# Kernel tuning notes

Hardware: AMD Instinct MI355X
Metric: run time of the kernel (lower is better)

The kernel has to match this reference:

```python
import jax, jax.numpy as jnp
import numpy as np

B, LV, LT, D, H = 32, 196, 40, 512, 8
DH = D // H


def setup_inputs() -> dict:
    key = jax.random.key(0)
    ks = jax.random.split(key, 10)
    s = 0.02
    return {
        "bef_feat": jax.random.normal(ks[0], (B, LV, D), jnp.float32),
        "sent_feat": jax.random.normal(ks[1], (B, LT, D), jnp.float32),
        "aft_feat": jax.random.normal(ks[2], (B, LV, D), jnp.float32),
        "masks": jnp.ones((B, LT), jnp.float32),
        "conv1_w": jax.random.normal(ks[3], (D, 2 * D), jnp.float32) * s,  # 1x1 conv: (out,in)
        "conv1_b": jnp.zeros((D,), jnp.float32),
        "in_proj_w": jax.random.normal(ks[4], (3 * D, D), jnp.float32) * s,
        "out_proj_w": jax.random.normal(ks[5], (D, D), jnp.float32) * s,
        "conv2_w": jax.random.normal(ks[6], (D, D), jnp.float32) * s,
        "conv2_b": jnp.zeros((D,), jnp.float32),
        "q_w": jax.random.normal(ks[7], (D, D), jnp.float32) * s,
        "q_b": jnp.zeros((D,), jnp.float32),
        "k_w": jax.random.normal(ks[8], (D, D), jnp.float32) * s,
        "k_b": jnp.zeros((D,), jnp.float32),
        "logit_scale": jnp.ones((), jnp.float32),
    }


def _forward(bef_feat, sent_feat, aft_feat, masks,
             conv1_w, conv1_b, in_proj_w, out_proj_w, conv2_w, conv2_b,
             q_w, q_b, k_w, k_b, logit_scale):
    batch, Lv, d = bef_feat.shape
    # masked text mean (plain mean over full length, as in original)
    sent = sent_feat * masks[:, :, None]
    sent_mean = jnp.mean(sent, axis=1)  # (B, D)
    # concat image grid feat with broadcast text feat -> 1x1 conv (conv1)
    img = jnp.transpose(bef_feat, (0, 2, 1))                       # (B, D, 196)
    txt = jnp.broadcast_to(sent_mean[:, :, None], (batch, d, Lv))  # (B, D, 196)
    v1 = jnp.concatenate([img, txt], axis=1)                       # (B, 2D, 196)
    v1 = jnp.einsum('bcl,oc->blo', v1, conv1_w) + conv1_b          # (B, 196, D)
    # multi-head self-attention over the 196 positions (no biases)
    qkv = jnp.einsum('bld,ed->ble', v1, in_proj_w)                 # (B, 196, 3D)
    q, k, v = jnp.split(qkv, 3, axis=-1)
    to_heads = lambda t: t.reshape(batch, Lv, H, DH).transpose(0, 2, 1, 3)
    q, k, v = to_heads(q), to_heads(k), to_heads(v)
    scores = jnp.einsum('bhld,bhmd->bhlm', q, k) / jnp.sqrt(jnp.float32(DH))
    attn = jax.nn.softmax(scores, axis=-1)
    o = jnp.einsum('bhlm,bhmd->bhld', attn, v)
    o = o.transpose(0, 2, 1, 3).reshape(batch, Lv, d)
    o = o @ out_proj_w.T
    # 1x1 conv (conv2)
    mod_img1 = jnp.einsum('bld,od->blo', o, conv2_w) + conv2_b     # (B, 196, D)
    # ContraAttention: cross-batch retrieval logits
    ql = (mod_img1 @ q_w.T + q_b).reshape(batch, Lv, H, DH).transpose(0, 2, 1, 3)  # (B,H,196,DH)
    kl = (aft_feat @ k_w.T + k_b).reshape(batch, Lv, H, DH).transpose(0, 2, 1, 3)  # (B,H,196,DH)
    logits = jnp.einsum('ahld,bhmd->ablm', ql, kl)                 # (B, B, 196, 196), sums over h,d
    # vid_mask and com_mask (attention_mask) are all-ones -> sums are Lv
    t2v = jnp.sum(jnp.max(logits, axis=-1), axis=2) / jnp.float32(Lv)  # (B, B)
    v2t = jnp.sum(jnp.max(logits, axis=-2), axis=2) / jnp.float32(Lv)  # (B, B)
    S = 0.5 * (t2v + v2t) * jnp.exp(logit_scale)
    cross_en = lambda m: -jnp.mean(jnp.diag(jax.nn.log_softmax(m, axis=-1)))
    return 0.5 * (cross_en(S) + cross_en(S.T))


def reference(bef_feat, sent_feat, aft_feat, masks,
              conv1_w, conv1_b, in_proj_w, out_proj_w, conv2_w, conv2_b,
              q_w, q_b, k_w, k_b, logit_scale):
    return _forward(bef_feat, sent_feat, aft_feat, masks,
                    conv1_w, conv1_b, in_proj_w, out_proj_w, conv2_w, conv2_b,
                    q_w, q_b, k_w, k_b, logit_scale)
```

## Files before the change

### kernel.cpp

```cpp
#include <hip/hip_runtime.h>


typedef unsigned int u32;
typedef unsigned short u16;
typedef __attribute__((ext_vector_type(8))) short bf16x8;
typedef __attribute__((ext_vector_type(4))) float f32x4;

#define DEV __device__ __forceinline__

DEV u16 f2bf(float f) {
  u32 u = __builtin_bit_cast(u32, f);
  u = (u + 0x7FFFu + ((u >> 16) & 1u)) >> 16;
  return (u16)u;
}
DEV float bf2f(u16 h) { u32 u = ((u32)h) << 16; return __builtin_bit_cast(float, u); }
DEV u32 encf(float f) { u32 u = __builtin_bit_cast(u32, f); return (u & 0x80000000u) ? ~u : (u | 0x80000000u); }
DEV float decf(u32 e) { u32 u = (e & 0x80000000u) ? (e & 0x7FFFFFFFu) : ~e; return __builtin_bit_cast(float, u); }

DEV void gll16(const u16* g, u16* l) {
  __builtin_amdgcn_global_load_lds(
      (const __attribute__((address_space(1))) void*)g,
      (__attribute__((address_space(3))) void*)l, 16, 0, 0);
}

#define VMCNT0 asm volatile("s_waitcnt vmcnt(0)" ::: "memory")
#define SBAR __builtin_amdgcn_s_barrier()

DEV void cast8(const float* __restrict__ in, u16* __restrict__ out, int i) {
  const float4* p = (const float4*)in + (size_t)i * 2;
  float4 a = p[0], b = p[1];
  u16 t[8] = {f2bf(a.x), f2bf(a.y), f2bf(a.z), f2bf(a.w),
              f2bf(b.x), f2bf(b.y), f2bf(b.z), f2bf(b.w)};
  *(uint4*)(out + (size_t)i * 8) = *(uint4*)t;
}

DEV void tcast(const float* __restrict__ in, u16* __restrict__ out, int t, int tid, float* sm) {
  int bx = t & 15, by = t >> 4;
  int tx = tid & 31, ty = tid >> 5;
  float (*tt)[33] = (float(*)[33])sm;
  for (int i = ty; i < 32; i += 8) tt[i][tx] = in[(size_t)(by * 32 + i) * 512 + bx * 32 + tx];
  __syncthreads();
  for (int i = ty; i < 32; i += 8) out[(size_t)(bx * 32 + i) * 512 + by * 32 + tx] = f2bf(tt[tx][i]);
}

__global__ __launch_bounds__(256) void k_prep(
    const float* __restrict__ bef, const float* __restrict__ aft,
    const float* __restrict__ sent, const float* __restrict__ masks,
    const float* __restrict__ conv1_w, const float* __restrict__ conv1_b,
    const float* __restrict__ in_proj_w, const float* __restrict__ out_proj_w,
    const float* __restrict__ conv2_w, const float* __restrict__ conv2_b,
    const float* __restrict__ q_w, const float* __restrict__ q_b,
    const float* __restrict__ k_w,
    u16* __restrict__ bef16, u16* __restrict__ aft16,
    u16* __restrict__ inproj16, u16* __restrict__ kw16, u16* __restrict__ qw16,
    u16* __restrict__ w1a16, u16* __restrict__ wcT16, u16* __restrict__ woT16,
    float* __restrict__ biasb, float* __restrict__ biasq,
    uint4* __restrict__ maxbuf) {
  __shared__ float smemf[1056];
  const int blk = blockIdx.x, tid = threadIdx.x;
  if (blk < 32) {
    int b = blk;
    float* sm = smemf;
    for (int d = tid; d < 512; d += 256) {
      float s = 0.f;
#pragma unroll 8
      for (int t = 0; t < 40; ++t) s += sent[(size_t)b * 40 * 512 + (size_t)t * 512 + d] * masks[b * 40 + t];
      sm[d] = s * (1.0f / 40.0f);
    }
    __syncthreads();
    for (int o = tid; o < 512; o += 256) {
      const float* wr = conv1_w + (size_t)o * 1024 + 512;
      float acc = conv1_b[o];
#pragma unroll 8
      for (int c = 0; c < 512; ++c) acc += sm[c] * wr[c];
      biasb[b * 512 + o] = acc;
    }
  } else if (blk < 424) {
    maxbuf[(size_t)(blk - 32) * 256 + tid] = (uint4){0u, 0u, 0u, 0u};
  } else if (blk < 426) {
    int j = (blk - 424) * 256 + tid;
    if (j < 512) {
      const float* wr = q_w + (size_t)j * 512;
      float acc = q_b[j];
#pragma unroll 8
      for (int d = 0; d < 512; ++d) acc += wr[d] * conv2_b[d];
      biasq[j] = acc;
    }
  } else if (blk < 1994) {
    cast8(bef, bef16, (blk - 426) * 256 + tid);
  } else if (blk < 3562) {
    cast8(aft, aft16, (blk - 1994) * 256 + tid);
  } else if (blk < 3946) {
    cast8(in_proj_w, inproj16, (blk - 3562) * 256 + tid);
  } else if (blk < 4074) {
    cast8(k_w, kw16, (blk - 3946) * 256 + tid);
  } else if (blk < 4202) {
    cast8(q_w, qw16, (blk - 4074) * 256 + tid);
  } else if (blk < 4330) {
    int i = (blk - 4202) * 256 + tid;
    int o = i >> 6, c0 = (i & 63) * 8;
    const float* p = conv1_w + (size_t)o * 1024 + c0;
    u16 t[8];
#pragma unroll
    for (int j = 0; j < 8; ++j) t[j] = f2bf(p[j]);
    *(uint4*)(w1a16 + (size_t)o * 512 + c0) = *(uint4*)t;
  } else if (blk < 4586) {
    tcast(conv2_w, wcT16, blk - 4330, tid, smemf);
  } else {
    tcast(out_proj_w, woT16, blk - 4586, tid, smemf);
  }
}

DEV void stage_g3(const u16* __restrict__ xb, const u16* __restrict__ wb,
                  u16* Xb, u16* Wb, int wave, int lane, int koff, int scol) {
  int r8 = lane >> 3;
#pragma unroll
  for (int i = 0; i < 8; ++i) {
    int s = wave + i * 4;
    if (s < 16) gll16(xb + (size_t)(s * 8 + r8) * 512 + koff + scol, Xb + s * 512);
    else        gll16(wb + (size_t)((s - 16) * 8 + r8) * 512 + koff + scol, Wb + (s - 16) * 512);
  }
}

DEV void comp_g3(const u16* Xb, const u16* Wb, int wr, int wc, int quad, int l15, int rsw,
                 f32x4 (&acc)[4][4]) {
#pragma unroll
  for (int kk = 0; kk < 64; kk += 32) {
    int co = (kk | (quad << 3)) ^ rsw;
    bf16x8 af[4];
#pragma unroll
    for (int s = 0; s < 4; ++s)
      af[s] = *(const bf16x8*)&Xb[(wr * 64 + s * 16 + l15) * 64 + co];
#pragma unroll
    for (int nt = 0; nt < 4; ++nt) {
      bf16x8 b = *(const bf16x8*)&Wb[(wc * 64 + nt * 16 + l15) * 64 + co];
#pragma unroll
      for (int s = 0; s < 4; ++s)
        acc[s][nt] = __builtin_amdgcn_mfma_f32_16x16x32_bf16(af[s], b, acc[s][nt], 0, 0, 0);
    }
  }
}

__global__ __launch_bounds__(256) void k_gemm3d(
    const u16* __restrict__ X1, const u16* __restrict__ W1, u16* __restrict__ o1,
    const float* __restrict__ b1, int nbx1, int N1, int m1, int nblk1,
    const u16* __restrict__ X2, const u16* __restrict__ W2, u16* __restrict__ o2,
    const float* __restrict__ b2, int nbx2, int N2, int m2) {
  __shared__ u16 Xl0[128 * 64], Xl1[128 * 64];
  __shared__ u16 Wl0[128 * 64], Wl1[128 * 64];
  int g = blockIdx.x;
  const u16 *X, *W; u16* out; const float* bias; int N, biasMode, bx, by;
  if (g < nblk1) {
    X = X1; W = W1; out = o1; bias = b1; N = N1; biasMode = m1;
    bx = g % nbx1; by = g / nbx1;
  } else {
    g -= nblk1;
    X = X2; W = W2; out = o2; bias = b2; N = N2; biasMode = m2;
    bx = g % nbx2; by = g / nbx2;
  }
  int tid = threadIdx.x;
  int tileM = bx * 128, tileN = by * 128;
  int wave = tid >> 6, lane = tid & 63, quad = lane >> 4, l15 = lane & 15;
  int wr = wave >> 1, wc = wave & 1;
  const int rsw = (l15 & 7) << 3;
  const int scol = (((lane & 7) ^ ((lane >> 3) & 7)) << 3);
  f32x4 z = {0.f, 0.f, 0.f, 0.f};
  f32x4 acc[4][4];
#pragma unroll
  for (int s = 0; s < 4; ++s)
#pragma unroll
    for (int nt = 0; nt < 4; ++nt) acc[s][nt] = z;
  const u16* xb = X + (size_t)tileM * 512;
  const u16* wb = W + (size_t)tileN * 512;

  stage_g3(xb, wb, Xl0, Wl0, wave, lane, 0, scol);
  VMCNT0; SBAR;
#pragma unroll
  for (int kc = 0; kc < 8; kc += 2) {
    stage_g3(xb, wb, Xl1, Wl1, wave, lane, (kc + 1) * 64, scol);
    comp_g3(Xl0, Wl0, wr, wc, quad, l15, rsw, acc);
    VMCNT0; SBAR;
    if (kc + 2 < 8)
      stage_g3(xb, wb, Xl0, Wl0, wave, lane, (kc + 2) * 64, scol);
    comp_g3(Xl1, Wl1, wr, wc, quad, l15, rsw, acc);
    VMCNT0; SBAR;
  }
#pragma unroll
  for (int s = 0; s < 4; ++s) {
    int row0 = tileM + wr * 64 + s * 16 + quad * 4;
#pragma unroll
    for (int nt = 0; nt < 4; ++nt) {
      int col = tileN + wc * 64 + nt * 16 + l15;
      float bv = (biasMode == 1) ? bias[col] : 0.0f;
#pragma unroll
      for (int r = 0; r < 4; ++r) {
        int row = row0 + r;
        float v = acc[s][nt][r] + bv;
        if (biasMode == 2) v += bias[(row / 196) * 512 + col];
        out[(size_t)row * N + col] = f2bf(v);
      }
    }
  }
}

__global__ __launch_bounds__(256, 1) void k_attn2(const u16* __restrict__ qkv, u16* __restrict__ o_out) {
  const int blk = blockIdx.x;
  const int b = blk >> 4, h = (blk >> 1) & 7, half = blk & 1;
  const int sb = half * 8, se = half ? 13 : 8;
  __shared__ u16 Ks[208 * 72];
  __shared__ u16 Vt[64 * 232];
  __shared__ u16 Ps[4][16 * 232];
  const int tid = threadIdx.x;
  const int wave = tid >> 6, lane = tid & 63, quad = lane >> 4, l15 = lane & 15;
  const size_t base = (size_t)b * 196 * 1536 + (size_t)h * 64;

  for (int i = tid; i < 64 * 232 / 4; i += 256) ((unsigned long long*)Vt)[i] = 0ULL;
  for (int i = tid; i < 4 * 16 * 24; i += 256) {
    int w = i / 384, rem = i - w * 384;
    int r = rem / 24, c = rem - r * 24;
    Ps[w][r * 232 + 208 + c] = 0;
  }
  __syncthreads();

  for (int idx = tid; idx < 208 * 8; idx += 256) {
    int r = idx >> 3, c = (idx & 7) * 8;
    uint4 v = {0, 0, 0, 0};
    if (r < 196) v = *(const uint4*)&qkv[base + 512 + (size_t)r * 1536 + c];
    *(uint4*)&Ks[r * 72 + c] = v;
  }
  for (int idx = tid; idx < 196 * 8; idx += 256) {
    int p = idx >> 3, f0 = (idx & 7) * 8;
    uint4 v = *(const uint4*)&qkv[base + 1024 + (size_t)p * 1536 + f0];
    u16 t[8]; *(uint4*)t = v;
#pragma unroll
    for (int j = 0; j < 8; ++j) Vt[(f0 + j) * 232 + p] = t[j];
  }
  bf16x8 qz = {0, 0, 0, 0, 0, 0, 0, 0};
  bf16x8 qf[2][2];
#pragma unroll
  for (int i = 0; i < 2; ++i) {
    int s = sb + wave + i * 4;
    int row = s * 16 + l15;
#pragma unroll
    for (int c = 0; c < 2; ++c) {
      bf16x8 v = qz;
      if (s < se && row < 196)
        v = *(const bf16x8*)&qkv[base + (size_t)row * 1536 + c * 32 + quad * 8];
      qf[i][c] = v;
    }
  }
  __syncthreads();

  const f32x4 z = {0.f, 0.f, 0.f, 0.f};
  for (int i = 0; i < 2; ++i) {
    int s = sb + wave + i * 4;
    if (s >= se) break;
    f32x4 acc[13];
#pragma unroll
    for (int nt = 0; nt < 13; ++nt) acc[nt] = z;
#pragma unroll
    for (int c = 0; c < 2; ++c) {
      bf16x8 a = qf[i][c];
#pragma unroll
      for (int nt = 0; nt < 13; ++nt) {
        bf16x8 bfr = *(const bf16x8*)&Ks[(nt * 16 + l15) * 72 + c * 32 + quad * 8];
        acc[nt] = __builtin_amdgcn_mfma_f32_16x16x32_bf16(a, bfr, acc[nt], 0, 0, 0);
      }
    }
#pragma unroll
    for (int r = 0; r < 4; ++r) {
      float m = -3e38f;
#pragma unroll
      for (int nt = 0; nt < 13; ++nt) {
        float sv = acc[nt][r] * 0.125f;
        acc[nt][r] = sv;
        if (nt < 12 || l15 < 4) m = fmaxf(m, sv);
      }
#pragma unroll
      for (int off = 1; off < 16; off <<= 1) m = fmaxf(m, __shfl_xor(m, off));
      float ssum = 0.f;
#pragma unroll
      for (int nt = 0; nt < 13; ++nt) {
        float p = (nt < 12 || l15 < 4) ? __expf(acc[nt][r] - m) : 0.f;
        acc[nt][r] = p;
        ssum += p;
      }
#pragma unroll
      for (int off = 1; off < 16; off <<= 1) ssum += __shfl_xor(ssum, off);
      float is = 1.0f / ssum;
      int row = quad * 4 + r;
#pragma unroll
      for (int nt = 0; nt < 13; ++nt) {
        float v = acc[nt][r] * is;
        float vx = __shfl_xor(v, 1);
        if ((l15 & 1) == 0) {
          u32 pk = (u32)f2bf(v) | ((u32)f2bf(vx) << 16);
          *(u32*)&Ps[wave][row * 232 + nt * 16 + l15] = pk;
        }
      }
    }
    f32x4 oacc[4] = {z, z, z, z};
#pragma unroll
    for (int kc = 0; kc < 7; ++kc) {
      bf16x8 a = *(const bf16x8*)&Ps[wave][l15 * 232 + kc * 32 + quad * 8];
#pragma unroll
      for (int nt = 0; nt < 4; ++nt) {
        bf16x8 bfr = *(const bf16x8*)&Vt[(nt * 16 + l15) * 232 + kc * 32 + quad * 8];
        oacc[nt] = __builtin_amdgcn_mfma_f32_16x16x32_bf16(a, bfr, oacc[nt], 0, 0, 0);
      }
    }
#pragma unroll
    for (int nt = 0; nt < 4; ++nt) {
#pragma unroll
      for (int r = 0; r < 4; ++r) {
        int row = s * 16 + quad * 4 + r;
        if (row < 196)
          o_out[((size_t)b * 196 + row) * 512 + h * 64 + nt * 16 + l15] = f2bf(oacc[nt][r]);
      }
    }
  }
}

DEV void stage_lg(const u16* __restrict__ qbase, const u16* __restrict__ kbase,
                  u16* Qb, u16* Kb, int wave, int lane, int koff, int scol) {
  int r4 = lane >> 2;
#pragma unroll
  for (int i = 0; i < 6; ++i) {
    int s = wave + i * 4;
    if (s < 8) {
      gll16(qbase + (size_t)(s * 16 + r4) * 512 + koff + scol, Qb + s * 512);
    } else if (s < 21) {
      int j = s - 8;
      int r = j * 16 + r4; if (r > 195) r = 195;
      gll16(kbase + (size_t)r * 512 + koff + scol, Kb + j * 512);
    }
  }
}

DEV void comp_lg(const u16* Qb, const u16* Kb, int wave, int l15, int co, f32x4 (&acc)[2][13]) {
  bf16x8 af0 = *(const bf16x8*)&Qb[(wave * 16 + l15) * 32 + co];
  bf16x8 af1 = *(const bf16x8*)&Qb[((wave + 4) * 16 + l15) * 32 + co];
  __builtin_amdgcn_s_setprio(1);
#pragma unroll
  for (int nt = 0; nt < 13; ++nt) {
    bf16x8 b = *(const bf16x8*)&Kb[(nt * 16 + l15) * 32 + co];
    acc[0][nt] = __builtin_amdgcn_mfma_f32_16x16x32_bf16(af0, b, acc[0][nt], 0, 0, 0);
    acc[1][nt] = __builtin_amdgcn_mfma_f32_16x16x32_bf16(af1, b, acc[1][nt], 0, 0, 0);
  }
  __builtin_amdgcn_s_setprio(0);
}

#define WAIT_W() do { \
    if (wave == 0) asm volatile("s_waitcnt vmcnt(6)" ::: "memory"); \
    else           asm volatile("s_waitcnt vmcnt(5)" ::: "memory"); \
  } while (0)

__global__ __launch_bounds__(256) void k_logits2(const u16* __restrict__ QL, const u16* __restrict__ KL,
                                                 u32* __restrict__ rowmax, u32* __restrict__ colmax) {
  int lin = blockIdx.y * 49 + blockIdx.x;
  lin = (lin & 7) * 196 + (lin >> 3);
  const int bx = lin % 49, b = lin / 49;
  const int row0 = bx * 128;
  __shared__ u16 Qb0[128 * 32], Qb1[128 * 32], Qb2[128 * 32];
  __shared__ u16 Kb0[208 * 32], Kb1[208 * 32], Kb2[208 * 32];
  __shared__ float colred[2][4 * 208];
  const int tid = threadIdx.x;
  const int wave = tid >> 6, lane = tid & 63, quad = lane >> 4, l15 = lane & 15;
  const int scol = (((lane & 3) ^ ((lane >> 3) & 3)) << 3);
  const int co = ((quad ^ ((l15 >> 1) & 3)) << 3);
  const int a0 = row0 / 196;
  const int lsplit = (a0 + 1) * 196 - row0;
  const f32x4 z = {0.f, 0.f, 0.f, 0.f};
  f32x4 acc[2][13];
#pragma unroll
  for (int s = 0; s < 2; ++s)
#pragma unroll
    for (int nt = 0; nt < 13; ++nt) acc[s][nt] = z;
  const u16* qbase = QL + (size_t)row0 * 512;
  const u16* kbase = KL + (size_t)b * 196 * 512;

  u16 *qa = Qb0, *qb = Qb1, *qc = Qb2;
  u16 *ka = Kb0, *kb = Kb1, *kc = Kb2;
  stage_lg(qbase, kbase, qa, ka, wave, lane, 0, scol);
  stage_lg(qbase, kbase, qb, kb, wave, lane, 32, scol);
  for (int t = 0; t < 14; ++t) {
    WAIT_W();
    SBAR;
    stage_lg(qbase, kbase, qc, kc, wave, lane, (t + 2) * 32, scol);
    comp_lg(qa, ka, wave, l15, co, acc);
    u16* tq = qa; qa = qb; qb = qc; qc = tq;
    u16* tk = ka; ka = kb; kb = kc; kc = tk;
  }
  WAIT_W(); SBAR;
  comp_lg(qa, ka, wave, l15, co, acc);
  { u16* tq = qa; qa = qb; qb = qc; qc = tq;
    u16* tk = ka; ka = kb; kb = kc; kc = tk; }
  VMCNT0; SBAR;
  comp_lg(qa, ka, wave, l15, co, acc);

#pragma unroll
  for (int s = 0; s < 2; ++s) {
#pragma unroll
    for (int r = 0; r < 4; ++r) {
      float m = -3e38f;
#pragma unroll
      for (int nt = 0; nt < 13; ++nt)
        if (nt < 12 || l15 < 4) m = fmaxf(m, acc[s][nt][r]);
#pragma unroll
      for (int off = 8; off > 0; off >>= 1) m = fmaxf(m, __shfl_xor(m, off, 16));
      if (l15 == 0) {
        int lr = (wave + s * 4) * 16 + quad * 4 + r;
        int aa = a0, ll = row0 - a0 * 196 + lr;
        if (ll >= 196) { aa += 1; ll -= 196; }
        atomicMax(&rowmax[((size_t)aa * 32 + b) * 196 + ll], encf(m));
      }
    }
  }
#pragma unroll
  for (int nt = 0; nt < 13; ++nt) {
    float cm0 = -3e38f, cm1 = -3e38f;
#pragma unroll
    for (int s = 0; s < 2; ++s)
#pragma unroll
      for (int r = 0; r < 4; ++r) {
        int lr = (wave + s * 4) * 16 + quad * 4 + r;
        float v = acc[s][nt][r];
        if (lr < lsplit) cm0 = fmaxf(cm0, v); else cm1 = fmaxf(cm1, v);
      }
    cm0 = fmaxf(cm0, __shfl_xor(cm0, 16)); cm0 = fmaxf(cm0, __shfl_xor(cm0, 32));
    cm1 = fmaxf(cm1, __shfl_xor(cm1, 16)); cm1 = fmaxf(cm1, __shfl_xor(cm1, 32));
    if (quad == 0) {
      colred[0][wave * 208 + nt * 16 + l15] = cm0;
      colred[1][wave * 208 + nt * 16 + l15] = cm1;
    }
  }
  __syncthreads();
  for (int c = tid; c < 196; c += 256) {
    float m0 = fmaxf(fmaxf(colred[0][c], colred[0][208 + c]), fmaxf(colred[0][416 + c], colred[0][624 + c]));
    atomicMax(&colmax[((size_t)a0 * 32 + b) * 196 + c], encf(m0));
    if (lsplit < 128) {
      float m1 = fmaxf(fmaxf(colred[1][c], colred[1][208 + c]), fmaxf(colred[1][416 + c], colred[1][624 + c]));
      atomicMax(&colmax[((size_t)(a0 + 1) * 32 + b) * 196 + c], encf(m1));
    }
  }
}

__global__ __launch_bounds__(256) void k_sred(const u32* __restrict__ maxbuf, float* __restrict__ Sws) {
  int wave = threadIdx.x >> 6, lane = threadIdx.x & 63;
  int p = blockIdx.x * 4 + wave;
  const u32* rp = maxbuf + (size_t)p * 196;
  const u32* cp = maxbuf + 200704 + (size_t)p * 196;
  float s = 0.f;
  for (int i = lane; i < 196; i += 64) s += decf(rp[i]) + decf(cp[i]);
#pragma unroll
  for (int off = 1; off < 64; off <<= 1) s += __shfl_xor(s, off);
  if (lane == 0) Sws[p] = s;
}

__global__ __launch_bounds__(1024) void k_final(const float* __restrict__ Sws,
                                                const float* __restrict__ logit_scale, float* __restrict__ out) {
  __shared__ float S[1024];
  __shared__ float terms[64];
  int tid = threadIdx.x;
  float sc = 0.5f * __expf(logit_scale[0]);
  S[tid] = sc * Sws[tid] * (1.0f / 196.0f);
  __syncthreads();
  if (tid < 64) {
    int aa = tid & 31;
    bool rowMode = tid < 32;
    float mx = -3e38f;
    for (int j = 0; j < 32; ++j) {
      float v = rowMode ? S[aa * 32 + j] : S[j * 32 + aa];
      mx = fmaxf(mx, v);
    }
    float se = 0.f;
    for (int j = 0; j < 32; ++j) {
      float v = rowMode ? S[aa * 32 + j] : S[j * 32 + aa];
      se += __expf(v - mx);
    }
    terms[tid] = S[aa * 33] - (mx + logf(se));
  }
  __syncthreads();
  if (tid == 0) {
    float s2 = 0.f;
    for (int i = 0; i < 64; ++i) s2 += terms[i];
    out[0] = -s2 * (1.0f / 64.0f);
  }
}

extern "C" void kernel_launch(void* const* d_in, const int* in_sizes, int n_in,
                              void* d_out, int out_size, void* d_ws, size_t ws_size,
                              hipStream_t stream) {
  const float* bef       = (const float*)d_in[0];
  const float* sent      = (const float*)d_in[1];
  const float* aft       = (const float*)d_in[2];
  const float* masks     = (const float*)d_in[3];
  const float* conv1_w   = (const float*)d_in[4];
  const float* conv1_b   = (const float*)d_in[5];
  const float* in_proj_w = (const float*)d_in[6];
  const float* out_proj_w= (const float*)d_in[7];
  const float* conv2_w   = (const float*)d_in[8];
  const float* conv2_b   = (const float*)d_in[9];
  const float* q_w       = (const float*)d_in[10];
  const float* q_b       = (const float*)d_in[11];
  const float* k_w       = (const float*)d_in[12];
  const float* k_b       = (const float*)d_in[13];
  const float* logit_scale = (const float*)d_in[14];
  float* out = (float*)d_out;

  char* ws = (char*)d_ws;
  size_t off = 0;
  auto alloc = [&](size_t bytes) -> char* {
    char* p = ws + off;
    off += (bytes + 255) & ~(size_t)255;
    return p;
  };
  const size_t MROWS = 32 * 196;
  u16* bef16    = (u16*)alloc(MROWS * 512 * 2);
  u16* aft16    = (u16*)alloc(MROWS * 512 * 2);
  u16* w1a16    = (u16*)alloc(512 * 512 * 2);
  u16* inproj16 = (u16*)alloc(1536 * 512 * 2);
  u16* kw16     = (u16*)alloc(512 * 512 * 2);
  u16* qw16     = (u16*)alloc(512 * 512 * 2);
  u16* wcT16    = (u16*)alloc(512 * 512 * 2);
  u16* woT16    = (u16*)alloc(512 * 512 * 2);
  u16* wt16     = (u16*)alloc(512 * 512 * 2);
  u16* wcomb16  = (u16*)alloc(512 * 512 * 2);
  float* biasb  = (float*)alloc(32 * 512 * 4);
  float* biasq  = (float*)alloc(512 * 4);
  u16* v116     = (u16*)alloc(MROWS * 512 * 2);
  u16* qkv16    = (u16*)alloc(MROWS * 1536 * 2);
  u16* oattn16  = (u16*)alloc(MROWS * 512 * 2);
  u16* QL16     = (u16*)alloc(MROWS * 512 * 2);
  u16* KL16     = (u16*)alloc(MROWS * 512 * 2);
  u32* maxbuf   = (u32*)alloc(2 * 32 * 32 * 196 * 4);
  float* Sws    = (float*)alloc(1024 * 4);
  u32* rowmax   = maxbuf;
  u32* colmax   = maxbuf + 32 * 32 * 196;

  k_prep<<<4842, 256, 0, stream>>>(bef, aft, sent, masks, conv1_w, conv1_b,
                                   in_proj_w, out_proj_w, conv2_w, conv2_b,
                                   q_w, q_b, k_w,
                                   bef16, aft16, inproj16, kw16, qw16,
                                   w1a16, wcT16, woT16, biasb, biasq,
                                   (uint4*)maxbuf);
  k_gemm3d<<<212, 256, 0, stream>>>(bef16, w1a16, v116, biasb, 49, 512, 2, 196,
                                    qw16, wcT16, wt16, nullptr, 4, 512, 0);
  k_gemm3d<<<604, 256, 0, stream>>>(v116, inproj16, qkv16, nullptr, 49, 1536, 0, 588,
                                    wt16, woT16, wcomb16, nullptr, 4, 512, 0);
  k_attn2<<<512, 256, 0, stream>>>(qkv16, oattn16);
  k_gemm3d<<<392, 256, 0, stream>>>(oattn16, wcomb16, QL16, biasq, 49, 512, 1, 196,
                                    aft16, kw16, KL16, k_b, 49, 512, 1);
  k_logits2<<<dim3(49, 32), 256, 0, stream>>>(QL16, KL16, rowmax, colmax);
  k_sred<<<256, 256, 0, stream>>>(maxbuf, Sws);
  k_final<<<1, 1024, 0, stream>>>(Sws, logit_scale, out);
}
```

Baseline: 331.8 us.

## Enlarge logits tile to 256 rows with 512 threads; remap gemm block order

The cross-batch logits kernel now processes 256 query rows per block with 8 waves, which halves the grid and doubles reuse of each staged K tile. The pipeline drops from triple to double buffering with full vmcnt(0) waits, and the column-max reduction now handles rows that span up to three batch items, with bounds checks on the last tile. The GEMM kernel also remaps block indices so the 8 groups of blocks that are interleaved round-robin (likely one per XCD) each receive a contiguous range of tiles, aiming for better L2 locality. In exchange, the simpler double buffer exposes more load latency, and the 512-thread blocks may run at lower occupancy.

```diff
diff --git a/kernel.cpp b/kernel.cpp
--- a/kernel.cpp
+++ b/kernel.cpp
@@ -149,6 +149,11 @@
   __shared__ u16 Xl0[128 * 64], Xl1[128 * 64];
   __shared__ u16 Wl0[128 * 64], Wl1[128 * 64];
   int g = blockIdx.x;
+  {
+    int nwg = gridDim.x, q = nwg >> 3, r = nwg & 7;
+    int x = g & 7, idx = g >> 3;
+    g = (x < r ? x * (q + 1) : r * (q + 1) + (x - r) * q) + idx;
+  }
   const u16 *X, *W; u16* out; const float* bias; int N, biasMode, bx, by;
   if (g < nblk1) {
     X = X1; W = W1; out = o1; bias = b1; N = N1; biasMode = m1;
@@ -321,25 +326,26 @@
   }
 }
 
-DEV void stage_lg(const u16* __restrict__ qbase, const u16* __restrict__ kbase,
+DEV void stage_l3(const u16* __restrict__ QL, const u16* __restrict__ kbase, int row0,
                   u16* Qb, u16* Kb, int wave, int lane, int koff, int scol) {
   int r4 = lane >> 2;
 #pragma unroll
-  for (int i = 0; i < 6; ++i) {
-    int s = wave + i * 4;
-    if (s < 8) {
-      gll16(qbase + (size_t)(s * 16 + r4) * 512 + koff + scol, Qb + s * 512);
-    } else if (s < 21) {
-      int j = s - 8;
+  for (int i = 0; i < 4; ++i) {
+    int s = wave + i * 8;
+    if (s < 16) {
+      int r = row0 + s * 16 + r4; if (r > 6271) r = 6271;
+      gll16(QL + (size_t)r * 512 + koff + scol, Qb + s * 512);
+    } else if (s < 29) {
+      int j = s - 16;
       int r = j * 16 + r4; if (r > 195) r = 195;
       gll16(kbase + (size_t)r * 512 + koff + scol, Kb + j * 512);
     }
   }
 }
 
-DEV void comp_lg(const u16* Qb, const u16* Kb, int wave, int l15, int co, f32x4 (&acc)[2][13]) {
-  bf16x8 af0 = *(const bf16x8*)&Qb[(wave * 16 + l15) * 32 + co];
-  bf16x8 af1 = *(const bf16x8*)&Qb[((wave + 4) * 16 + l15) * 32 + co];
+DEV void comp_l3(const u16* Qb, const u16* Kb, int wave, int l15, int co, f32x4 (&acc)[2][13]) {
+  bf16x8 af0 = *(const bf16x8*)&Qb[(wave * 32 + l15) * 32 + co];
+  bf16x8 af1 = *(const bf16x8*)&Qb[(wave * 32 + 16 + l15) * 32 + co];
   __builtin_amdgcn_s_setprio(1);
 #pragma unroll
   for (int nt = 0; nt < 13; ++nt) {
@@ -350,54 +356,41 @@
   __builtin_amdgcn_s_setprio(0);
 }
 
-#define WAIT_W() do { \
-    if (wave == 0) asm volatile("s_waitcnt vmcnt(6)" ::: "memory"); \
-    else           asm volatile("s_waitcnt vmcnt(5)" ::: "memory"); \
-  } while (0)
-
-__global__ __launch_bounds__(256) void k_logits2(const u16* __restrict__ QL, const u16* __restrict__ KL,
-                                                 u32* __restrict__ rowmax, u32* __restrict__ colmax) {
-  int lin = blockIdx.y * 49 + blockIdx.x;
-  lin = (lin & 7) * 196 + (lin >> 3);
-  const int bx = lin % 49, b = lin / 49;
-  const int row0 = bx * 128;
-  __shared__ u16 Qb0[128 * 32], Qb1[128 * 32], Qb2[128 * 32];
-  __shared__ u16 Kb0[208 * 32], Kb1[208 * 32], Kb2[208 * 32];
-  __shared__ float colred[2][4 * 208];
+__global__ __launch_bounds__(512, 4) void k_logits2(const u16* __restrict__ QL, const u16* __restrict__ KL,
+                                                    u32* __restrict__ rowmax, u32* __restrict__ colmax) {
+  int lin = blockIdx.y * 25 + blockIdx.x;
+  lin = (lin & 7) * 100 + (lin >> 3);
+  const int bx = lin % 25, b = lin / 25;
+  const int row0 = bx * 256;
+  __shared__ u16 Qb0[256 * 32], Qb1[256 * 32];
+  __shared__ u16 Kb0[208 * 32], Kb1[208 * 32];
+  __shared__ float colred[3][8][208];
   const int tid = threadIdx.x;
   const int wave = tid >> 6, lane = tid & 63, quad = lane >> 4, l15 = lane & 15;
   const int scol = (((lane & 3) ^ ((lane >> 3) & 3)) << 3);
   const int co = ((quad ^ ((l15 >> 1) & 3)) << 3);
   const int a0 = row0 / 196;
-  const int lsplit = (a0 + 1) * 196 - row0;
+  const int lsplit1 = (a0 + 1) * 196 - row0;
+  const int lsplit2 = lsplit1 + 196;
   const f32x4 z = {0.f, 0.f, 0.f, 0.f};
   f32x4 acc[2][13];
 #pragma unroll
   for (int s = 0; s < 2; ++s)
 #pragma unroll
     for (int nt = 0; nt < 13; ++nt) acc[s][nt] = z;
-  const u16* qbase = QL + (size_t)row0 * 512;
   const u16* kbase = KL + (size_t)b * 196 * 512;
 
-  u16 *qa = Qb0, *qb = Qb1, *qc = Qb2;
-  u16 *ka = Kb0, *kb = Kb1, *kc = Kb2;
-  stage_lg(qbase, kbase, qa, ka, wave, lane, 0, scol);
-  stage_lg(qbase, kbase, qb, kb, wave, lane, 32, scol);
-  for (int t = 0; t < 14; ++t) {
-    WAIT_W();
-    SBAR;
-    stage_lg(qbase, kbase, qc, kc, wave, lane, (t + 2) * 32, scol);
-    comp_lg(qa, ka, wave, l15, co, acc);
-    u16* tq = qa; qa = qb; qb = qc; qc = tq;
-    u16* tk = ka; ka = kb; kb = kc; kc = tk;
-  }
-  WAIT_W(); SBAR;
-  comp_lg(qa, ka, wave, l15, co, acc);
-  { u16* tq = qa; qa = qb; qb = qc; qc = tq;
-    u16* tk = ka; ka = kb; kb = kc; kc = tk; }
+  stage_l3(QL, kbase, row0, Qb0, Kb0, wave, lane, 0, scol);
   VMCNT0; SBAR;
-  comp_lg(qa, ka, wave, l15, co, acc);
-
+  for (int kc = 0; kc < 16; kc += 2) {
+    stage_l3(QL, kbase, row0, Qb1, Kb1, wave, lane, (kc + 1) * 32, scol);
+    comp_l3(Qb0, Kb0, wave, l15, co, acc);
+    VMCNT0; SBAR;
+    if (kc + 2 < 16)
+      stage_l3(QL, kbase, row0, Qb0, Kb0, wave, lane, (kc + 2) * 32, scol);
+    comp_l3(Qb1, Kb1, wave, l15, co, acc);
+    VMCNT0; SBAR;
+  }
 #pragma unroll
   for (int s = 0; s < 2; ++s) {
 #pragma unroll
@@ -409,38 +402,54 @@
 #pragma unroll
       for (int off = 8; off > 0; off >>= 1) m = fmaxf(m, __shfl_xor(m, off, 16));
       if (l15 == 0) {
-        int lr = (wave + s * 4) * 16 + quad * 4 + r;
+        int lr = wave * 32 + s * 16 + quad * 4 + r;
         int aa = a0, ll = row0 - a0 * 196 + lr;
         if (ll >= 196) { aa += 1; ll -= 196; }
-        atomicMax(&rowmax[((size_t)aa * 32 + b) * 196 + ll], encf(m));
+        if (ll >= 196) { aa += 1; ll -= 196; }
+        if (aa < 32)
+          atomicMax(&rowmax[((size_t)aa * 32 + b) * 196 + ll], encf(m));
       }
     }
   }
 #pragma unroll
   for (int nt = 0; nt < 13; ++nt) {
-    float cm0 = -3e38f, cm1 = -3e38f;
+    float cm0 = -3e38f, cm1 = -3e38f, cm2 = -3e38f;
 #pragma unroll
     for (int s = 0; s < 2; ++s)
 #pragma unroll
       for (int r = 0; r < 4; ++r) {
-        int lr = (wave + s * 4) * 16 + quad * 4 + r;
+        int lr = wave * 32 + s * 16 + quad * 4 + r;
         float v = acc[s][nt][r];
-        if (lr < lsplit) cm0 = fmaxf(cm0, v); else cm1 = fmaxf(cm1, v);
+        if (lr < lsplit1) cm0 = fmaxf(cm0, v);
+        else if (lr < lsplit2) cm1 = fmaxf(cm1, v);
+        else cm2 = fmaxf(cm2, v);
       }
     cm0 = fmaxf(cm0, __shfl_xor(cm0, 16)); cm0 = fmaxf(cm0, __shfl_xor(cm0, 32));
     cm1 = fmaxf(cm1, __shfl_xor(cm1, 16)); cm1 = fmaxf(cm1, __shfl_xor(cm1, 32));
+    cm2 = fmaxf(cm2, __shfl_xor(cm2, 16)); cm2 = fmaxf(cm2, __shfl_xor(cm2, 32));
     if (quad == 0) {
-      colred[0][wave * 208 + nt * 16 + l15] = cm0;
-      colred[1][wave * 208 + nt * 16 + l15] = cm1;
+      colred[0][wave][nt * 16 + l15] = cm0;
+      colred[1][wave][nt * 16 + l15] = cm1;
+      colred[2][wave][nt * 16 + l15] = cm2;
     }
   }
   __syncthreads();
-  for (int c = tid; c < 196; c += 256) {
-    float m0 = fmaxf(fmaxf(colred[0][c], colred[0][208 + c]), fmaxf(colred[0][416 + c], colred[0][624 + c]));
+  for (int c = tid; c < 196; c += 512) {
+    float m0 = colred[0][0][c];
+#pragma unroll
+    for (int w = 1; w < 8; ++w) m0 = fmaxf(m0, colred[0][w][c]);
     atomicMax(&colmax[((size_t)a0 * 32 + b) * 196 + c], encf(m0));
-    if (lsplit < 128) {
-      float m1 = fmaxf(fmaxf(colred[1][c], colred[1][208 + c]), fmaxf(colred[1][416 + c], colred[1][624 + c]));
+    if (a0 + 1 < 32) {
+      float m1 = colred[1][0][c];
+#pragma unroll
+      for (int w = 1; w < 8; ++w) m1 = fmaxf(m1, colred[1][w][c]);
       atomicMax(&colmax[((size_t)(a0 + 1) * 32 + b) * 196 + c], encf(m1));
+    }
+    if (lsplit2 < 256 && a0 + 2 < 32) {
+      float m2 = colred[2][0][c];
+#pragma unroll
+      for (int w = 1; w < 8; ++w) m2 = fmaxf(m2, colred[2][w][c]);
+      atomicMax(&colmax[((size_t)(a0 + 2) * 32 + b) * 196 + c], encf(m2));
     }
   }
 }
@@ -551,7 +560,7 @@
   k_attn2<<<512, 256, 0, stream>>>(qkv16, oattn16);
   k_gemm3d<<<392, 256, 0, stream>>>(oattn16, wcomb16, QL16, biasq, 49, 512, 1, 196,
                                     aft16, kw16, KL16, k_b, 49, 512, 1);
-  k_logits2<<<dim3(49, 32), 256, 0, stream>>>(QL16, KL16, rowmax, colmax);
+  k_logits2<<<dim3(25, 32), 512, 0, stream>>>(QL16, KL16, rowmax, colmax);
   k_sred<<<256, 256, 0, stream>>>(maxbuf, Sws);
   k_final<<<1, 1024, 0, stream>>>(Sws, logit_scale, out);
 }
```

Result: slower. 390.0 us (+17.6%).

## Split logits kernel across key-column halves with double-buffered staging

Applied to the files above, without the earlier changes.

The cross-batch logits kernel now splits each 128-row block's 196 key columns into two halves (7 and 6 tiles), doubling the grid to 98x32 blocks. This uses fewer accumulators and less LDS per block. The pipeline also changes from a triple buffer with partial vmcnt waits to a double buffer that waits for all loads before each barrier. More blocks should improve occupancy and load balance, but the Q tile is now loaded twice, the full waits expose more load latency, and there are more atomic max writes.

```diff
diff --git a/kernel.cpp b/kernel.cpp
--- a/kernel.cpp
+++ b/kernel.cpp
@@ -321,91 +321,72 @@
   }
 }
 
-DEV void stage_lg(const u16* __restrict__ qbase, const u16* __restrict__ kbase,
-                  u16* Qb, u16* Kb, int wave, int lane, int koff, int scol) {
-  int r4 = lane >> 2;
-#pragma unroll
-  for (int i = 0; i < 6; ++i) {
-    int s = wave + i * 4;
-    if (s < 8) {
-      gll16(qbase + (size_t)(s * 16 + r4) * 512 + koff + scol, Qb + s * 512);
-    } else if (s < 21) {
-      int j = s - 8;
-      int r = j * 16 + r4; if (r > 195) r = 195;
-      gll16(kbase + (size_t)r * 512 + koff + scol, Kb + j * 512);
-    }
-  }
-}
-
-DEV void comp_lg(const u16* Qb, const u16* Kb, int wave, int l15, int co, f32x4 (&acc)[2][13]) {
-  bf16x8 af0 = *(const bf16x8*)&Qb[(wave * 16 + l15) * 32 + co];
-  bf16x8 af1 = *(const bf16x8*)&Qb[((wave + 4) * 16 + l15) * 32 + co];
-  __builtin_amdgcn_s_setprio(1);
-#pragma unroll
-  for (int nt = 0; nt < 13; ++nt) {
-    bf16x8 b = *(const bf16x8*)&Kb[(nt * 16 + l15) * 32 + co];
-    acc[0][nt] = __builtin_amdgcn_mfma_f32_16x16x32_bf16(af0, b, acc[0][nt], 0, 0, 0);
-    acc[1][nt] = __builtin_amdgcn_mfma_f32_16x16x32_bf16(af1, b, acc[1][nt], 0, 0, 0);
-  }
-  __builtin_amdgcn_s_setprio(0);
-}
-
-#define WAIT_W() do { \
-    if (wave == 0) asm volatile("s_waitcnt vmcnt(6)" ::: "memory"); \
-    else           asm volatile("s_waitcnt vmcnt(5)" ::: "memory"); \
-  } while (0)
-
-__global__ __launch_bounds__(256) void k_logits2(const u16* __restrict__ QL, const u16* __restrict__ KL,
-                                                 u32* __restrict__ rowmax, u32* __restrict__ colmax) {
-  int lin = blockIdx.y * 49 + blockIdx.x;
-  lin = (lin & 7) * 196 + (lin >> 3);
-  const int bx = lin % 49, b = lin / 49;
-  const int row0 = bx * 128;
-  __shared__ u16 Qb0[128 * 32], Qb1[128 * 32], Qb2[128 * 32];
-  __shared__ u16 Kb0[208 * 32], Kb1[208 * 32], Kb2[208 * 32];
-  __shared__ float colred[2][4 * 208];
-  const int tid = threadIdx.x;
+template<int NTB, int NT>
+DEV void lg_body(const u16* __restrict__ QL, const u16* __restrict__ KL,
+                 u32* __restrict__ rowmax, u32* __restrict__ colmax,
+                 u16* Qb0, u16* Qb1, u16* Kb0, u16* Kb1,
+                 float (&colred)[2][4][112],
+                 int row0, int b, int tid) {
   const int wave = tid >> 6, lane = tid & 63, quad = lane >> 4, l15 = lane & 15;
   const int scol = (((lane & 3) ^ ((lane >> 3) & 3)) << 3);
   const int co = ((quad ^ ((l15 >> 1) & 3)) << 3);
   const int a0 = row0 / 196;
   const int lsplit = (a0 + 1) * 196 - row0;
-  const f32x4 z = {0.f, 0.f, 0.f, 0.f};
-  f32x4 acc[2][13];
-#pragma unroll
-  for (int s = 0; s < 2; ++s)
-#pragma unroll
-    for (int nt = 0; nt < 13; ++nt) acc[s][nt] = z;
+  const int r4 = lane >> 2;
   const u16* qbase = QL + (size_t)row0 * 512;
   const u16* kbase = KL + (size_t)b * 196 * 512;
-
-  u16 *qa = Qb0, *qb = Qb1, *qc = Qb2;
-  u16 *ka = Kb0, *kb = Kb1, *kc = Kb2;
-  stage_lg(qbase, kbase, qa, ka, wave, lane, 0, scol);
-  stage_lg(qbase, kbase, qb, kb, wave, lane, 32, scol);
-  for (int t = 0; t < 14; ++t) {
-    WAIT_W();
-    SBAR;
-    stage_lg(qbase, kbase, qc, kc, wave, lane, (t + 2) * 32, scol);
-    comp_lg(qa, ka, wave, l15, co, acc);
-    u16* tq = qa; qa = qb; qb = qc; qc = tq;
-    u16* tk = ka; ka = kb; kb = kc; kc = tk;
-  }
-  WAIT_W(); SBAR;
-  comp_lg(qa, ka, wave, l15, co, acc);
-  { u16* tq = qa; qa = qb; qb = qc; qc = tq;
-    u16* tk = ka; ka = kb; kb = kc; kc = tk; }
+  const f32x4 z = {0.f, 0.f, 0.f, 0.f};
+  f32x4 acc[2][NT];
+#pragma unroll
+  for (int s = 0; s < 2; ++s)
+#pragma unroll
+    for (int nt = 0; nt < NT; ++nt) acc[s][nt] = z;
+
+  auto STAGE = [&](u16* Qb, u16* Kb, int koff) {
+#pragma unroll
+    for (int i = 0; i < 4; ++i) {
+      int s = wave + i * 4;
+      if (s < 8) {
+        gll16(qbase + (size_t)(s * 16 + r4) * 512 + koff + scol, Qb + s * 512);
+      } else if (s < 8 + NT) {
+        int j = s - 8;
+        int gr = NTB * 16 + j * 16 + r4; if (gr > 195) gr = 195;
+        gll16(kbase + (size_t)gr * 512 + koff + scol, Kb + j * 512);
+      }
+    }
+  };
+  auto COMP = [&](const u16* Qb, const u16* Kb) {
+    bf16x8 af0 = *(const bf16x8*)&Qb[(wave * 16 + l15) * 32 + co];
+    bf16x8 af1 = *(const bf16x8*)&Qb[((wave + 4) * 16 + l15) * 32 + co];
+    __builtin_amdgcn_s_setprio(1);
+#pragma unroll
+    for (int nt = 0; nt < NT; ++nt) {
+      bf16x8 bf = *(const bf16x8*)&Kb[(nt * 16 + l15) * 32 + co];
+      acc[0][nt] = __builtin_amdgcn_mfma_f32_16x16x32_bf16(af0, bf, acc[0][nt], 0, 0, 0);
+      acc[1][nt] = __builtin_amdgcn_mfma_f32_16x16x32_bf16(af1, bf, acc[1][nt], 0, 0, 0);
+    }
+    __builtin_amdgcn_s_setprio(0);
+  };
+
+  STAGE(Qb0, Kb0, 0);
   VMCNT0; SBAR;
-  comp_lg(qa, ka, wave, l15, co, acc);
-
+  for (int kc = 0; kc < 16; kc += 2) {
+    STAGE(Qb1, Kb1, (kc + 1) * 32);
+    COMP(Qb0, Kb0);
+    VMCNT0; SBAR;
+    if (kc + 2 < 16)
+      STAGE(Qb0, Kb0, (kc + 2) * 32);
+    COMP(Qb1, Kb1);
+    VMCNT0; SBAR;
+  }
 #pragma unroll
   for (int s = 0; s < 2; ++s) {
 #pragma unroll
     for (int r = 0; r < 4; ++r) {
       float m = -3e38f;
 #pragma unroll
-      for (int nt = 0; nt < 13; ++nt)
-        if (nt < 12 || l15 < 4) m = fmaxf(m, acc[s][nt][r]);
+      for (int nt = 0; nt < NT; ++nt)
+        if (NTB + nt < 12 || l15 < 4) m = fmaxf(m, acc[s][nt][r]);
 #pragma unroll
       for (int off = 8; off > 0; off >>= 1) m = fmaxf(m, __shfl_xor(m, off, 16));
       if (l15 == 0) {
@@ -417,7 +398,7 @@
     }
   }
 #pragma unroll
-  for (int nt = 0; nt < 13; ++nt) {
+  for (int nt = 0; nt < NT; ++nt) {
     float cm0 = -3e38f, cm1 = -3e38f;
 #pragma unroll
     for (int s = 0; s < 2; ++s)
@@ -430,19 +411,41 @@
     cm0 = fmaxf(cm0, __shfl_xor(cm0, 16)); cm0 = fmaxf(cm0, __shfl_xor(cm0, 32));
     cm1 = fmaxf(cm1, __shfl_xor(cm1, 16)); cm1 = fmaxf(cm1, __shfl_xor(cm1, 32));
     if (quad == 0) {
-      colred[0][wave * 208 + nt * 16 + l15] = cm0;
-      colred[1][wave * 208 + nt * 16 + l15] = cm1;
+      colred[0][wave][nt * 16 + l15] = cm0;
+      colred[1][wave][nt * 16 + l15] = cm1;
     }
   }
   __syncthreads();
-  for (int c = tid; c < 196; c += 256) {
-    float m0 = fmaxf(fmaxf(colred[0][c], colred[0][208 + c]), fmaxf(colred[0][416 + c], colred[0][624 + c]));
-    atomicMax(&colmax[((size_t)a0 * 32 + b) * 196 + c], encf(m0));
-    if (lsplit < 128) {
-      float m1 = fmaxf(fmaxf(colred[1][c], colred[1][208 + c]), fmaxf(colred[1][416 + c], colred[1][624 + c]));
-      atomicMax(&colmax[((size_t)(a0 + 1) * 32 + b) * 196 + c], encf(m1));
-    }
-  }
+  for (int c = tid; c < NT * 16; c += 256) {
+    int gcol = NTB * 16 + c;
+    if (gcol < 196) {
+      float m0 = fmaxf(fmaxf(colred[0][0][c], colred[0][1][c]),
+                       fmaxf(colred[0][2][c], colred[0][3][c]));
+      atomicMax(&colmax[((size_t)a0 * 32 + b) * 196 + gcol], encf(m0));
+      if (lsplit < 128) {
+        float m1 = fmaxf(fmaxf(colred[1][0][c], colred[1][1][c]),
+                         fmaxf(colred[1][2][c], colred[1][3][c]));
+        atomicMax(&colmax[((size_t)(a0 + 1) * 32 + b) * 196 + gcol], encf(m1));
+      }
+    }
+  }
+}
+
+__global__ __launch_bounds__(256) void k_logits2(const u16* __restrict__ QL, const u16* __restrict__ KL,
+                                                 u32* __restrict__ rowmax, u32* __restrict__ colmax) {
+  int lin = blockIdx.y * 98 + blockIdx.x;
+  lin = (lin & 7) * 392 + (lin >> 3);
+  const int half = lin & 1;
+  const int rest = lin >> 1;
+  const int bx = rest % 49, b = rest / 49;
+  const int row0 = bx * 128;
+  __shared__ u16 Qb0[128 * 32], Qb1[128 * 32];
+  __shared__ u16 Kb0[112 * 32], Kb1[112 * 32];
+  __shared__ float colred[2][4][112];
+  if (half == 0)
+    lg_body<0, 7>(QL, KL, rowmax, colmax, Qb0, Qb1, Kb0, Kb1, colred, row0, b, (int)threadIdx.x);
+  else
+    lg_body<7, 6>(QL, KL, rowmax, colmax, Qb0, Qb1, Kb0, Kb1, colred, row0, b, (int)threadIdx.x);
 }
 
 __global__ __launch_bounds__(256) void k_sred(const u32* __restrict__ maxbuf, float* __restrict__ Sws) {
@@ -551,7 +554,7 @@
   k_attn2<<<512, 256, 0, stream>>>(qkv16, oattn16);
   k_gemm3d<<<392, 256, 0, stream>>>(oattn16, wcomb16, QL16, biasq, 49, 512, 1, 196,
                                     aft16, kw16, KL16, k_b, 49, 512, 1);
-  k_logits2<<<dim3(49, 32), 256, 0, stream>>>(QL16, KL16, rowmax, colmax);
+  k_logits2<<<dim3(98, 32), 256, 0, stream>>>(QL16, KL16, rowmax, colmax);
   k_sred<<<256, 256, 0, stream>>>(maxbuf, Sws);
   k_final<<<1, 1024, 0, stream>>>(Sws, logit_scale, out);
 }
```

Result: slower. 349.2 us (+5.3%).

## Load Q fragments straight to registers and double-buffer only K in logits

Applied to the files above, without the earlier changes.

The cross-batch logits kernel no longer stages Q tiles through LDS. Each wave reads its Q MFMA fragments directly from global memory into registers, and only K tiles pass through LDS via global_load_lds, now in two buffers instead of three. This removes Q LDS traffic and cuts LDS footprint, which may allow more resident blocks. In exchange the pipeline is shallower: it waits on vmcnt(0) plus a barrier after every K-chunk, and the direct Q loads are strided 16-byte reads that expose global latency.

```diff
diff --git a/kernel.cpp b/kernel.cpp
--- a/kernel.cpp
+++ b/kernel.cpp
@@ -321,53 +321,19 @@
   }
 }
 
-DEV void stage_lg(const u16* __restrict__ qbase, const u16* __restrict__ kbase,
-                  u16* Qb, u16* Kb, int wave, int lane, int koff, int scol) {
-  int r4 = lane >> 2;
-#pragma unroll
-  for (int i = 0; i < 6; ++i) {
-    int s = wave + i * 4;
-    if (s < 8) {
-      gll16(qbase + (size_t)(s * 16 + r4) * 512 + koff + scol, Qb + s * 512);
-    } else if (s < 21) {
-      int j = s - 8;
-      int r = j * 16 + r4; if (r > 195) r = 195;
-      gll16(kbase + (size_t)r * 512 + koff + scol, Kb + j * 512);
-    }
-  }
-}
-
-DEV void comp_lg(const u16* Qb, const u16* Kb, int wave, int l15, int co, f32x4 (&acc)[2][13]) {
-  bf16x8 af0 = *(const bf16x8*)&Qb[(wave * 16 + l15) * 32 + co];
-  bf16x8 af1 = *(const bf16x8*)&Qb[((wave + 4) * 16 + l15) * 32 + co];
-  __builtin_amdgcn_s_setprio(1);
-#pragma unroll
-  for (int nt = 0; nt < 13; ++nt) {
-    bf16x8 b = *(const bf16x8*)&Kb[(nt * 16 + l15) * 32 + co];
-    acc[0][nt] = __builtin_amdgcn_mfma_f32_16x16x32_bf16(af0, b, acc[0][nt], 0, 0, 0);
-    acc[1][nt] = __builtin_amdgcn_mfma_f32_16x16x32_bf16(af1, b, acc[1][nt], 0, 0, 0);
-  }
-  __builtin_amdgcn_s_setprio(0);
-}
-
-#define WAIT_W() do { \
-    if (wave == 0) asm volatile("s_waitcnt vmcnt(6)" ::: "memory"); \
-    else           asm volatile("s_waitcnt vmcnt(5)" ::: "memory"); \
-  } while (0)
-
 __global__ __launch_bounds__(256) void k_logits2(const u16* __restrict__ QL, const u16* __restrict__ KL,
                                                  u32* __restrict__ rowmax, u32* __restrict__ colmax) {
   int lin = blockIdx.y * 49 + blockIdx.x;
   lin = (lin & 7) * 196 + (lin >> 3);
   const int bx = lin % 49, b = lin / 49;
   const int row0 = bx * 128;
-  __shared__ u16 Qb0[128 * 32], Qb1[128 * 32], Qb2[128 * 32];
-  __shared__ u16 Kb0[208 * 32], Kb1[208 * 32], Kb2[208 * 32];
+  __shared__ u16 Kb0[208 * 32], Kb1[208 * 32];
   __shared__ float colred[2][4 * 208];
   const int tid = threadIdx.x;
   const int wave = tid >> 6, lane = tid & 63, quad = lane >> 4, l15 = lane & 15;
   const int scol = (((lane & 3) ^ ((lane >> 3) & 3)) << 3);
   const int co = ((quad ^ ((l15 >> 1) & 3)) << 3);
+  const int r4 = lane >> 2;
   const int a0 = row0 / 196;
   const int lsplit = (a0 + 1) * 196 - row0;
   const f32x4 z = {0.f, 0.f, 0.f, 0.f};
@@ -376,28 +342,49 @@
   for (int s = 0; s < 2; ++s)
 #pragma unroll
     for (int nt = 0; nt < 13; ++nt) acc[s][nt] = z;
-  const u16* qbase = QL + (size_t)row0 * 512;
   const u16* kbase = KL + (size_t)b * 196 * 512;
-
-  u16 *qa = Qb0, *qb = Qb1, *qc = Qb2;
-  u16 *ka = Kb0, *kb = Kb1, *kc = Kb2;
-  stage_lg(qbase, kbase, qa, ka, wave, lane, 0, scol);
-  stage_lg(qbase, kbase, qb, kb, wave, lane, 32, scol);
-  for (int t = 0; t < 14; ++t) {
-    WAIT_W();
-    SBAR;
-    stage_lg(qbase, kbase, qc, kc, wave, lane, (t + 2) * 32, scol);
-    comp_lg(qa, ka, wave, l15, co, acc);
-    u16* tq = qa; qa = qb; qb = qc; qc = tq;
-    u16* tk = ka; ka = kb; kb = kc; kc = tk;
-  }
-  WAIT_W(); SBAR;
-  comp_lg(qa, ka, wave, l15, co, acc);
-  { u16* tq = qa; qa = qb; qb = qc; qc = tq;
-    u16* tk = ka; ka = kb; kb = kc; kc = tk; }
+  const u16* qrowA = QL + (size_t)(row0 + wave * 16 + l15) * 512 + quad * 8;
+  const u16* qrowB = QL + (size_t)(row0 + (wave + 4) * 16 + l15) * 512 + quad * 8;
+
+  auto STAGEK = [&](u16* Kb, int koff) {
+#pragma unroll
+    for (int i = 0; i < 4; ++i) {
+      int s = wave + i * 4;
+      if (s < 13) {
+        int r = s * 16 + r4; if (r > 195) r = 195;
+        gll16(kbase + (size_t)r * 512 + koff + scol, Kb + s * 512);
+      }
+    }
+  };
+  auto COMP = [&](const u16* Kb, bf16x8 af0, bf16x8 af1) {
+    __builtin_amdgcn_s_setprio(1);
+#pragma unroll
+    for (int nt = 0; nt < 13; ++nt) {
+      bf16x8 bf = *(const bf16x8*)&Kb[(nt * 16 + l15) * 32 + co];
+      acc[0][nt] = __builtin_amdgcn_mfma_f32_16x16x32_bf16(af0, bf, acc[0][nt], 0, 0, 0);
+      acc[1][nt] = __builtin_amdgcn_mfma_f32_16x16x32_bf16(af1, bf, acc[1][nt], 0, 0, 0);
+    }
+    __builtin_amdgcn_s_setprio(0);
+  };
+
+  STAGEK(Kb0, 0);
+  bf16x8 qA0 = *(const bf16x8*)qrowA;
+  bf16x8 qA1 = *(const bf16x8*)qrowB;
   VMCNT0; SBAR;
-  comp_lg(qa, ka, wave, l15, co, acc);
-
+  for (int kc = 0; kc < 16; kc += 2) {
+    STAGEK(Kb1, (kc + 1) * 32);
+    bf16x8 qB0 = *(const bf16x8*)(qrowA + (kc + 1) * 32);
+    bf16x8 qB1 = *(const bf16x8*)(qrowB + (kc + 1) * 32);
+    COMP(Kb0, qA0, qA1);
+    VMCNT0; SBAR;
+    if (kc + 2 < 16) {
+      STAGEK(Kb0, (kc + 2) * 32);
+      qA0 = *(const bf16x8*)(qrowA + (kc + 2) * 32);
+      qA1 = *(const bf16x8*)(qrowB + (kc + 2) * 32);
+    }
+    COMP(Kb1, qB0, qB1);
+    VMCNT0; SBAR;
+  }
 #pragma unroll
   for (int s = 0; s < 2; ++s) {
 #pragma unroll
```

New measurement: 410.9 us. +23.8%, slower.
